# Optimization experiments

Hardware: AMD Instinct MI355X
Metric: run time of the kernel (lower is better)

Reference implementation:

```python
import jax, jax.numpy as jnp
import numpy as np

B = 16384      # batch of samples (vmap dim over the per-sample __call__)
L = 256        # latent_size: number of independent 1->16->1 MLPs
H = 16         # width_size of each MLP

def setup_inputs() -> dict:
    key = jax.random.key(0)
    k_y, k_w1, k_b1, k_w2, k_b2 = jax.random.split(key, 5)
    y = jax.random.normal(k_y, (B, L), dtype=jnp.float32)
    # Stacked parameters of the L independent eqx.nn.MLP(1,16,1,depth=1) nets.
    # Layer 1: Linear(1 -> 16): weight [L,H] (in_size=1 squeezed), bias [L,H]
    # Layer 2: Linear(16 -> 1): weight [L,H], bias [L]
    lim1 = 1.0  # eqx Linear init ~ U(-1/sqrt(in), 1/sqrt(in)); in=1 -> 1
    lim2 = 1.0 / np.sqrt(H)
    W1 = jax.random.uniform(k_w1, (L, H), minval=-lim1, maxval=lim1, dtype=jnp.float32)
    b1 = jax.random.uniform(k_b1, (L, H), minval=-lim1, maxval=lim1, dtype=jnp.float32)
    W2 = jax.random.uniform(k_w2, (L, H), minval=-lim2, maxval=lim2, dtype=jnp.float32)
    b2 = jax.random.uniform(k_b2, (L,), minval=-lim2, maxval=lim2, dtype=jnp.float32)
    return {"t": 0, "y": y, "W1": W1, "b1": b1, "W2": W2, "b2": b2, "args": 0}

def reference(t, y, W1, b1, W2, b2, args):
    # Batched/stacked form of: for each latent dim l,
    #   out_l = sigmoid(W2_l @ softplus(W1_l * y_l + b1_l) + b2_l)
    h = jax.nn.softplus(y[:, :, None] * W1[None, :, :] + b1[None, :, :])  # [B,L,H]
    out = jax.nn.sigmoid(jnp.einsum('blh,lh->bl', h, W2) + b2[None, :])   # [B,L]
    return out
```

## Files before the change

kernel.cpp:

```cpp
#include <hip/hip_runtime.h>
#include <hip/hip_bf16.h>

#define BB 16384
#define LL 256
#define HH 16
#define LO (-6.0f)
#define HI (6.0f)
#define NI 256
#define NE 257
#define LT 32
#define RP 16

static __device__ __forceinline__ float fast_exp2(float x) { return __builtin_amdgcn_exp2f(x); }
static __device__ __forceinline__ float fast_log2(float x) { return __builtin_amdgcn_logf(x); }

static __device__ __forceinline__ float mlp_exact(
    float yv, int l,
    const float* __restrict__ W1, const float* __restrict__ b1,
    const float* __restrict__ W2, const float* __restrict__ b2) {
    const float LOG2E = 1.4426950408889634f;
    float acc2 = b2[l] * LOG2E;
    #pragma unroll
    for (int h = 0; h < HH; ++h) {
        float x2 = fmaf(yv, W1[l * HH + h] * LOG2E, b1[l * HH + h] * LOG2E);
        float e  = fast_exp2(-fabsf(x2));
        float sp = fmaxf(x2, 0.0f) + fast_log2(1.0f + e);
        acc2 = fmaf(sp, W2[l * HH + h], acc2);
    }
    return __builtin_amdgcn_rcpf(1.0f + fast_exp2(-acc2));
}

__global__ __launch_bounds__(256) void build_lut(
    const float* __restrict__ W1, const float* __restrict__ b1,
    const float* __restrict__ W2, const float* __restrict__ b2,
    float* __restrict__ tbl) {
    const float LOG2E = 1.4426950408889634f;
    int gid = blockIdx.x * 256 + threadIdx.x;
    int entry = gid >> 2;
    int q = gid & 3;
    if (entry >= LL * NE) return;
    int l = entry / NE;
    int i = entry - l * NE;
    float u = LO + (HI - LO) * ((float)i / (float)NI);

    float part = 0.0f;
    #pragma unroll
    for (int hh = 0; hh < 4; ++hh) {
        int h = q * 4 + hh;
        float x2 = fmaf(u, W1[l * HH + h] * LOG2E, b1[l * HH + h] * LOG2E);
        float e  = fast_exp2(-fabsf(x2));
        float sp = fmaxf(x2, 0.0f) + fast_log2(1.0f + e);
        part = fmaf(sp, W2[l * HH + h], part);
    }
    part += __shfl_xor(part, 1, 64);
    part += __shfl_xor(part, 2, 64);
    if (q == 0) {
        float acc2 = part + b2[l] * LOG2E;
        tbl[entry] = __builtin_amdgcn_rcpf(1.0f + fast_exp2(-acc2));
    }
}

__global__ __launch_bounds__(256, 4) void lut_kernel(
    const float* __restrict__ y, float* __restrict__ out,
    const float* __restrict__ tbl,
    const float* __restrict__ W1, const float* __restrict__ b1,
    const float* __restrict__ W2, const float* __restrict__ b2) {
    __shared__ float s[LT * NE];
    const int lt = blockIdx.x & 7;
    const int bb = blockIdx.x >> 3;
    const int l0 = lt * LT;
    for (int j = threadIdx.x; j < LT * NE; j += 256)
        s[j] = tbl[l0 * NE + j];
    __syncthreads();

    const int l_local = threadIdx.x & (LT - 1);
    const int b_idx   = threadIdx.x >> 5;
    const int l       = l0 + l_local;
    const float* __restrict__ srow = s + l_local * NE;
    const float SCALE = (float)NI / (HI - LO);

    int b = bb * (RP * 8) + b_idx;
    #pragma unroll 4
    for (int r = 0; r < RP; ++r, b += 8) {
        float yv = y[b * LL + l];
        float t = (yv - LO) * SCALE;
        t = fminf(fmaxf(t, 0.0f), (float)NI);
        int i = (int)t;
        i = min(i, NI - 1);
        float fr = t - (float)i;
        float v0 = srow[i];
        float v1 = srow[i + 1];
        float res = fmaf(fr, v1 - v0, v0);
        if (__builtin_expect(fabsf(yv) > HI, 0)) {
            res = mlp_exact(yv, l, W1, b1, W2, b2);
        }
        out[b * LL + l] = res;
    }
}

extern "C" void kernel_launch(void* const* d_in, const int* in_sizes, int n_in,
                              void* d_out, int out_size, void* d_ws, size_t ws_size,
                              hipStream_t stream) {
    const float* y  = (const float*)d_in[1];
    const float* W1 = (const float*)d_in[2];
    const float* b1 = (const float*)d_in[3];
    const float* W2 = (const float*)d_in[4];
    const float* b2 = (const float*)d_in[5];
    float* out = (float*)d_out;
    float* tbl = (float*)d_ws;

    build_lut<<<(LL * NE * 4 + 255) / 256, 256, 0, stream>>>(W1, b1, W2, b2, tbl);
    lut_kernel<<<8 * (BB / (RP * 8)), 256, 0, stream>>>(y, out, tbl, W1, b1, W2, b2);
}
```

Before: 88.17 us.

## Replace LUT interpolation with fused exact per-element MLP evaluation

Drops the two-kernel lookup-table scheme (table build plus interpolated lookup from shared memory) in favour of one kernel. Each thread holds one latent's 48 weights in registers and evaluates the full 16-wide softplus MLP exactly for 16 batch rows. This removes the table-build launch, the shared-memory staging and the branchy fallback path, in exchange for many more transcendental instructions per element.

```diff
diff --git a/kernel.cpp b/kernel.cpp
--- a/kernel.cpp
+++ b/kernel.cpp
@@ -1,100 +1,51 @@
 #include <hip/hip_runtime.h>
-#include <hip/hip_bf16.h>
 
 #define BB 16384
 #define LL 256
 #define HH 16
-#define LO (-6.0f)
-#define HI (6.0f)
-#define NI 256
-#define NE 257
-#define LT 32
-#define RP 16
+#define RS 16
 
 static __device__ __forceinline__ float fast_exp2(float x) { return __builtin_amdgcn_exp2f(x); }
 static __device__ __forceinline__ float fast_log2(float x) { return __builtin_amdgcn_logf(x); }
 
-static __device__ __forceinline__ float mlp_exact(
-    float yv, int l,
+__global__ __launch_bounds__(256) void fused_mlp(
+    const float* __restrict__ y, float* __restrict__ out,
     const float* __restrict__ W1, const float* __restrict__ b1,
-    const float* __restrict__ W2, const float* __restrict__ b2) {
+    const float* __restrict__ W2, const float* __restrict__ b2)
+{
     const float LOG2E = 1.4426950408889634f;
-    float acc2 = b2[l] * LOG2E;
+    const int l = threadIdx.x;
+
+    float w1[HH], c1[HH], w2[HH];
+    const float4* __restrict__ W1v = reinterpret_cast<const float4*>(W1 + l * HH);
+    const float4* __restrict__ b1v = reinterpret_cast<const float4*>(b1 + l * HH);
+    const float4* __restrict__ W2v = reinterpret_cast<const float4*>(W2 + l * HH);
     #pragma unroll
-    for (int h = 0; h < HH; ++h) {
-        float x2 = fmaf(yv, W1[l * HH + h] * LOG2E, b1[l * HH + h] * LOG2E);
-        float e  = fast_exp2(-fabsf(x2));
-        float sp = fmaxf(x2, 0.0f) + fast_log2(1.0f + e);
-        acc2 = fmaf(sp, W2[l * HH + h], acc2);
+    for (int q = 0; q < HH / 4; ++q) {
+        float4 a = W1v[q], c = b1v[q], d = W2v[q];
+        w1[q * 4 + 0] = a.x * LOG2E; w1[q * 4 + 1] = a.y * LOG2E;
+        w1[q * 4 + 2] = a.z * LOG2E; w1[q * 4 + 3] = a.w * LOG2E;
+        c1[q * 4 + 0] = c.x * LOG2E; c1[q * 4 + 1] = c.y * LOG2E;
+        c1[q * 4 + 2] = c.z * LOG2E; c1[q * 4 + 3] = c.w * LOG2E;
+        w2[q * 4 + 0] = d.x; w2[q * 4 + 1] = d.y;
+        w2[q * 4 + 2] = d.z; w2[q * 4 + 3] = d.w;
     }
-    return __builtin_amdgcn_rcpf(1.0f + fast_exp2(-acc2));
-}
+    const float a2 = b2[l] * LOG2E;
 
-__global__ __launch_bounds__(256) void build_lut(
-    const float* __restrict__ W1, const float* __restrict__ b1,
-    const float* __restrict__ W2, const float* __restrict__ b2,
-    float* __restrict__ tbl) {
-    const float LOG2E = 1.4426950408889634f;
-    int gid = blockIdx.x * 256 + threadIdx.x;
-    int entry = gid >> 2;
-    int q = gid & 3;
-    if (entry >= LL * NE) return;
-    int l = entry / NE;
-    int i = entry - l * NE;
-    float u = LO + (HI - LO) * ((float)i / (float)NI);
-
-    float part = 0.0f;
-    #pragma unroll
-    for (int hh = 0; hh < 4; ++hh) {
-        int h = q * 4 + hh;
-        float x2 = fmaf(u, W1[l * HH + h] * LOG2E, b1[l * HH + h] * LOG2E);
-        float e  = fast_exp2(-fabsf(x2));
-        float sp = fmaxf(x2, 0.0f) + fast_log2(1.0f + e);
-        part = fmaf(sp, W2[l * HH + h], part);
-    }
-    part += __shfl_xor(part, 1, 64);
-    part += __shfl_xor(part, 2, 64);
-    if (q == 0) {
-        float acc2 = part + b2[l] * LOG2E;
-        tbl[entry] = __builtin_amdgcn_rcpf(1.0f + fast_exp2(-acc2));
-    }
-}
-
-__global__ __launch_bounds__(256, 4) void lut_kernel(
-    const float* __restrict__ y, float* __restrict__ out,
-    const float* __restrict__ tbl,
-    const float* __restrict__ W1, const float* __restrict__ b1,
-    const float* __restrict__ W2, const float* __restrict__ b2) {
-    __shared__ float s[LT * NE];
-    const int lt = blockIdx.x & 7;
-    const int bb = blockIdx.x >> 3;
-    const int l0 = lt * LT;
-    for (int j = threadIdx.x; j < LT * NE; j += 256)
-        s[j] = tbl[l0 * NE + j];
-    __syncthreads();
-
-    const int l_local = threadIdx.x & (LT - 1);
-    const int b_idx   = threadIdx.x >> 5;
-    const int l       = l0 + l_local;
-    const float* __restrict__ srow = s + l_local * NE;
-    const float SCALE = (float)NI / (HI - LO);
-
-    int b = bb * (RP * 8) + b_idx;
-    #pragma unroll 4
-    for (int r = 0; r < RP; ++r, b += 8) {
-        float yv = y[b * LL + l];
-        float t = (yv - LO) * SCALE;
-        t = fminf(fmaxf(t, 0.0f), (float)NI);
-        int i = (int)t;
-        i = min(i, NI - 1);
-        float fr = t - (float)i;
-        float v0 = srow[i];
-        float v1 = srow[i + 1];
-        float res = fmaf(fr, v1 - v0, v0);
-        if (__builtin_expect(fabsf(yv) > HI, 0)) {
-            res = mlp_exact(yv, l, W1, b1, W2, b2);
+    const int b0 = blockIdx.x * RS;
+    #pragma unroll 2
+    for (int r = 0; r < RS; ++r) {
+        float yv = y[(b0 + r) * LL + l];
+        float acc = a2;
+        #pragma unroll
+        for (int h = 0; h < HH; ++h) {
+            float x2 = fmaf(yv, w1[h], c1[h]);
+            float e  = fast_exp2(-fabsf(x2));
+            float sp = fmaxf(x2, 0.0f) + fast_log2(1.0f + e);
+            acc = fmaf(sp, w2[h], acc);
         }
-        out[b * LL + l] = res;
+        out[(b0 + r) * LL + l] =
+            __builtin_amdgcn_rcpf(1.0f + fast_exp2(-acc));
     }
 }
 
@@ -106,9 +57,7 @@
     const float* b1 = (const float*)d_in[3];
     const float* W2 = (const float*)d_in[4];
     const float* b2 = (const float*)d_in[5];
-    float* out = (float*)d_out;
-    float* tbl = (float*)d_ws;
+    (void)d_ws; (void)ws_size;
 
-    build_lut<<<(LL * NE * 4 + 255) / 256, 256, 0, stream>>>(W1, b1, W2, b2, tbl);
-    lut_kernel<<<8 * (BB / (RP * 8)), 256, 0, stream>>>(y, out, tbl, W1, b1, W2, b2);
+    fused_mlp<<<BB / RS, 256, 0, stream>>>(y, (float*)d_out, W1, b1, W2, b2);
 }
```

Measured after the change: 98.83 us. 12.1% more time.
